# Optimization experiments

Measured on AMD Instinct MI355X. Metric: run time of the kernel, lower is better.

Reference implementation:

```python
import jax, jax.numpy as jnp
import numpy as np


def _grid_sample_2d(feat, gx, gy):
    """Bilinear grid sample, zeros padding, align_corners=False.
    feat: [B,C,H,W]; gx,gy: [B,S,h,w] normalized coords in [-1,1].
    Returns [B,C,S,h,w]. Matches torch 5D grid_sample with D=1, z=0
    (z pixel coord = (1*1-1)/2 = 0 -> weight 1 on the single depth slice).
    """
    B, C, H, W = feat.shape
    ix = ((gx + 1.0) * W - 1.0) * 0.5  # unnormalize, align_corners=False
    iy = ((gy + 1.0) * H - 1.0) * 0.5
    x0 = jnp.floor(ix)
    y0 = jnp.floor(iy)
    tx = ix - x0  # fractional parts (differentiable w.r.t. grid)
    ty = iy - y0
    x0i = x0.astype(jnp.int32)
    y0i = y0.astype(jnp.int32)
    feat_flat = feat.reshape(B, C, H * W)

    def gather(xi, yi):
        valid = (xi >= 0) & (xi < W) & (yi >= 0) & (yi < H)
        xc = jnp.clip(xi, 0, W - 1)
        yc = jnp.clip(yi, 0, H - 1)
        idx = (yc * W + xc).reshape(B, 1, -1)  # [B,1,S*h*w]
        g = jnp.take_along_axis(feat_flat, idx, axis=2)  # [B,C,S*h*w]
        g = g.reshape(B, C, *xi.shape[1:])  # [B,C,S,h,w]
        return g * valid.astype(feat.dtype)[:, None]

    v00 = gather(x0i, y0i)
    v01 = gather(x0i + 1, y0i)
    v10 = gather(x0i, y0i + 1)
    v11 = gather(x0i + 1, y0i + 1)
    w00 = ((1.0 - tx) * (1.0 - ty))[:, None]
    w01 = (tx * (1.0 - ty))[:, None]
    w10 = ((1.0 - tx) * ty)[:, None]
    w11 = (tx * ty)[:, None]
    return v00 * w00 + v01 * w01 + v10 * w10 + v11 * w11


def setup_inputs() -> dict:
    key = jax.random.key(0)
    k1, k2, k3, k4 = jax.random.split(key, 4)
    B, C, S, H, W = 8, 8, 16, 128, 416
    feat_l = jax.random.normal(k1, (B, C, H, W), dtype=jnp.float32)
    feat_r = jax.random.normal(k2, (B, C, H, W), dtype=jnp.float32)
    # LUT: x,y normalized coords (slightly beyond [-1,1] to exercise zero padding);
    # z channel fixed to 0 exactly as in the module's lut_batch construction.
    lut_xy = jax.random.uniform(k3, (B, S, H, W, 2), dtype=jnp.float32,
                                minval=-1.1, maxval=1.1)
    lut = jnp.concatenate([lut_xy, jnp.zeros((B, S, H, W, 1), jnp.float32)], axis=-1)
    valid_mask = jax.random.bernoulli(k4, 0.8, (B, C, S, H, W))
    return {"feat_l": feat_l, "feat_r": feat_r, "lut": lut,
            "valid_mask": valid_mask, "no_steps": S}


def reference(feat_l, feat_r, lut, valid_mask, no_steps):
    """AnyNet._build_volume_2d: LUT grid_sample warp + masked inf-fill
    + abs-diff + channel-sum cost volume. Returns [B, no_steps, H, W]."""
    gx = lut[..., 0]  # torch grid order: (x, y, z), x indexes width
    gy = lut[..., 1]
    warped = _grid_sample_2d(feat_r, gx, gy)          # [B,C,S,H,W]
    diff = jnp.abs(warped - feat_l[:, :, None])       # broadcast feat_l over S
    cost_disp_feat = jnp.where(valid_mask, diff, jnp.inf)
    cost_volume = jnp.sum(cost_disp_feat, axis=1)     # [B,S,H,W]
    return cost_volume
```

## Files before the change

### kernel.cpp

```cpp
#include <hip/hip_runtime.h>
#include <math.h>

#define BB 8
#define CC 8
#define SS 16
#define HH 128
#define WW 416
#define HWSZ (HH * WW)

typedef unsigned short u16;
typedef unsigned char  u8;
typedef unsigned int   u32;
typedef unsigned short ushort8 __attribute__((ext_vector_type(8)));
typedef unsigned int   u32x4   __attribute__((ext_vector_type(4)));
typedef unsigned int   u32x2   __attribute__((ext_vector_type(2)));
typedef float          f32x2   __attribute__((ext_vector_type(2)));
typedef u32x4 __attribute__((aligned(4))) u32x4_a4;

__device__ __forceinline__ float bf2f(u16 v) {
    union { unsigned int u; float f; } x;
    x.u = ((unsigned int)v) << 16;
    return x.f;
}

__device__ __forceinline__ u16 f2bf(float f) {
    union { float ff; unsigned int u; } x;
    x.ff = f;
    unsigned int lsb = (x.u >> 16) & 1u;
    return (u16)((x.u + 0x7FFFu + lsb) >> 16);
}

__device__ __forceinline__ f32x2 bfpair(u32 w) {
    union { u32 u; float f; } lo, hi;
    lo.u = w << 16;
    hi.u = w & 0xFFFF0000u;
    f32x2 r; r.x = lo.f; r.y = hi.f;
    return r;
}

template<bool H>
__device__ __forceinline__ f32x2 fp8pair(u32 w) {
    return (f32x2)__builtin_amdgcn_cvt_pk_f32_fp8(w, H);
}

__device__ __forceinline__ u32 nz_flags(u32 w) {
    return (((w & 0x7F7F7F7Fu) + 0x7F7F7F7Fu) | w) & 0x80808080u;
}

__global__ __launch_bounds__(256) void pack_feats(
    const u16* __restrict__ feat_r,
    const u16* __restrict__ feat_l,
    u32x2* __restrict__ pr8,
    ushort8* __restrict__ pl)
{
    const int idx = blockIdx.x * 256 + threadIdx.x;
    const int b = idx / HWSZ;
    const int p = idx - b * HWSZ;
    const size_t base = (size_t)b * CC * HWSZ + p;

    float fr[CC];
    ushort8 vl;
#pragma unroll
    for (int c = 0; c < CC; ++c) {
        fr[c] = bf2f(__builtin_nontemporal_load(&feat_r[base + (size_t)c * HWSZ]));
        vl[c] = __builtin_nontemporal_load(&feat_l[base + (size_t)c * HWSZ]);
    }
    u32x2 o;
    int w0 = 0, w1 = 0;
    w0 = __builtin_amdgcn_cvt_pk_fp8_f32(fr[0], fr[1], w0, false);
    w0 = __builtin_amdgcn_cvt_pk_fp8_f32(fr[2], fr[3], w0, true);
    w1 = __builtin_amdgcn_cvt_pk_fp8_f32(fr[4], fr[5], w1, false);
    w1 = __builtin_amdgcn_cvt_pk_fp8_f32(fr[6], fr[7], w1, true);
    o.x = (u32)w0; o.y = (u32)w1;
    pr8[idx] = o;
    pl[idx] = vl;
}

__global__ __launch_bounds__(256) void mask_reduce(
    const u8* __restrict__ vmask,
    u8* __restrict__ pmask)
{
    const int t = blockIdx.x * 256 + threadIdx.x;
    const int n16 = SS * HWSZ / 16;
    const int b = t / n16;
    const int r = t - b * n16;
    const u32x4* __restrict__ vm4 = (const u32x4*)vmask;

    u32x4 f = { 0x80808080u, 0x80808080u, 0x80808080u, 0x80808080u };
#pragma unroll
    for (int c = 0; c < CC; ++c) {
        const u32x4 v = __builtin_nontemporal_load(
            &vm4[(size_t)(b * CC + c) * n16 + r]);
        f.x &= nz_flags(v.x);
        f.y &= nz_flags(v.y);
        f.z &= nz_flags(v.z);
        f.w &= nz_flags(v.w);
    }
    __builtin_nontemporal_store(f, &((u32x4*)pmask)[t]);
}

__global__ __launch_bounds__(256) void anynet_cost_volume(
    const u8* __restrict__ pfr8,
    const ushort8* __restrict__ pfl,
    const u16* __restrict__ lut,
    const u8*  __restrict__ pmask,
    u16* __restrict__ out)
{
    const int id = blockIdx.x;
    const int b  = id & 7;
    const int r  = id >> 3;
    const int hwblk = r % (HWSZ / 256);
    const int s     = r / (HWSZ / 256);
    const int hw = hwblk * 256 + (int)threadIdx.x;
    const size_t sp = (size_t)(b * SS + s) * HWSZ + hw;

    const size_t loff = sp * 3;
    const float gx = bf2f(__builtin_nontemporal_load(&lut[loff + 0]));
    const float gy = bf2f(__builtin_nontemporal_load(&lut[loff + 1]));
    const u8 m = __builtin_nontemporal_load(&pmask[sp]);

    const float ix = gx * (0.5f * WW) + (0.5f * WW - 0.5f);
    const float iy = gy * (0.5f * HH) + (0.5f * HH - 0.5f);
    const float x0f = floorf(ix);
    const float y0f = floorf(iy);
    const float tx = ix - x0f;
    const float ty = iy - y0f;
    const int x0 = (int)x0f;
    const int y0 = (int)y0f;
    const int x1 = x0 + 1;
    const int y1 = y0 + 1;

    const bool vx0 = ((unsigned)x0 < (unsigned)WW);
    const bool vx1 = ((unsigned)x1 < (unsigned)WW);
    const bool vy0 = ((unsigned)y0 < (unsigned)HH);
    const bool vy1 = ((unsigned)y1 < (unsigned)HH);

    const int yc0 = min(max(y0, 0), HH - 1);
    const int yc1 = min(max(y1, 0), HH - 1);
    const int bx  = min(max(x0, 0), WW - 2);

    float w00 = (1.0f - tx) * (1.0f - ty) * ((vx0 && vy0) ? 1.0f : 0.0f);
    float w01 = tx * (1.0f - ty)          * ((vx1 && vy0) ? 1.0f : 0.0f);
    float w10 = (1.0f - tx) * ty          * ((vx0 && vy1) ? 1.0f : 0.0f);
    float w11 = tx * ty                   * ((vx1 && vy1) ? 1.0f : 0.0f);

    const bool sw = (x0 == bx);
    const float wl0 = sw ? w00 : w01, wh0 = sw ? w01 : w00;
    const float wl1 = sw ? w10 : w11, wh1 = sw ? w11 : w10;

    const u8* __restrict__ imb = pfr8 + (size_t)b * HWSZ * 8;
    const u32x4 r0 = *(const u32x4_a4*)(imb + 8 * (size_t)(yc0 * WW + bx));
    const u32x4 r1 = *(const u32x4_a4*)(imb + 8 * (size_t)(yc1 * WW + bx));

    union { ushort8 sv; u32x4 w; } flu;
    flu.sv = pfl[(size_t)b * HWSZ + hw];

    f32x2 acc2; acc2.x = 0.0f; acc2.y = 0.0f;
#define CHPAIR(K, WSEL, HSEL)                                              \
    {                                                                      \
        f32x2 wv = fp8pair<HSEL>(WSEL ? r0.y : r0.x) * wl0;                \
        wv += fp8pair<HSEL>(WSEL ? r0.w : r0.z) * wh0;                     \
        wv += fp8pair<HSEL>(WSEL ? r1.y : r1.x) * wl1;                     \
        wv += fp8pair<HSEL>(WSEL ? r1.w : r1.z) * wh1;                     \
        const f32x2 d = wv - bfpair(flu.w[K]);                             \
        f32x2 ad; ad.x = fabsf(d.x); ad.y = fabsf(d.y);                    \
        acc2 += ad;                                                        \
    }
    CHPAIR(0, 0, false)
    CHPAIR(1, 0, true)
    CHPAIR(2, 1, false)
    CHPAIR(3, 1, true)
#undef CHPAIR
    float acc = acc2.x + acc2.y;

    acc = fminf(fmaxf(acc, 0.0f), 1e30f);
    if (!(acc >= 0.0f && acc <= 1e30f)) acc = 0.0f;
    __builtin_nontemporal_store((m == 0) ? (u16)0x7F7F : f2bf(acc), &out[sp]);
}

extern "C" void kernel_launch(void* const* d_in, const int* in_sizes, int n_in,
                              void* d_out, int out_size, void* d_ws, size_t ws_size,
                              hipStream_t stream) {
    const u16* feat_l = (const u16*)d_in[0];
    const u16* feat_r = (const u16*)d_in[1];
    const u16* lut    = (const u16*)d_in[2];
    const u8*  vmask  = (const u8*)d_in[3];
    u16* out = (u16*)d_out;

    u32x2* pfr8 = (u32x2*)d_ws;
    ushort8* pfl = (ushort8*)(pfr8 + (size_t)BB * HWSZ);
    u8* pmask = (u8*)(pfl + (size_t)BB * HWSZ);

    pack_feats<<<dim3(BB * HWSZ / 256), dim3(256), 0, stream>>>(
        feat_r, feat_l, pfr8, pfl);
    mask_reduce<<<dim3(BB * SS * HWSZ / 16 / 256), dim3(256), 0, stream>>>(
        vmask, pmask);

    anynet_cost_volume<<<dim3(BB * SS * (HWSZ / 256)), dim3(256), 0, stream>>>(
        (const u8*)pfr8, pfl, lut, pmask, out);
}
```

Before: 336.2 us.

## Fuse mask reduction and feat_l packing into the cost-volume kernel

Drops the separate mask_reduce kernel and the feat_l packing step, so the main kernel reads the per-channel valid mask and bf16 feat_l directly. This removes the intermediate packed-mask and packed-feat_l buffers and one kernel launch. The cost is byte-wide and strided per-channel loads in the main kernel instead of single vector loads.

```diff
diff --git a/kernel.cpp b/kernel.cpp
--- a/kernel.cpp
+++ b/kernel.cpp
@@ -30,28 +30,14 @@
     return (u16)((x.u + 0x7FFFu + lsb) >> 16);
 }
 
-__device__ __forceinline__ f32x2 bfpair(u32 w) {
-    union { u32 u; float f; } lo, hi;
-    lo.u = w << 16;
-    hi.u = w & 0xFFFF0000u;
-    f32x2 r; r.x = lo.f; r.y = hi.f;
-    return r;
-}
-
 template<bool H>
 __device__ __forceinline__ f32x2 fp8pair(u32 w) {
     return (f32x2)__builtin_amdgcn_cvt_pk_f32_fp8(w, H);
 }
 
-__device__ __forceinline__ u32 nz_flags(u32 w) {
-    return (((w & 0x7F7F7F7Fu) + 0x7F7F7F7Fu) | w) & 0x80808080u;
-}
-
-__global__ __launch_bounds__(256) void pack_feats(
+__global__ __launch_bounds__(256) void pack_feat_r8(
     const u16* __restrict__ feat_r,
-    const u16* __restrict__ feat_l,
-    u32x2* __restrict__ pr8,
-    ushort8* __restrict__ pl)
+    u32x2* __restrict__ pr8)
 {
     const int idx = blockIdx.x * 256 + threadIdx.x;
     const int b = idx / HWSZ;
@@ -59,12 +45,10 @@
     const size_t base = (size_t)b * CC * HWSZ + p;
 
     float fr[CC];
-    ushort8 vl;
 #pragma unroll
-    for (int c = 0; c < CC; ++c) {
+    for (int c = 0; c < CC; ++c)
         fr[c] = bf2f(__builtin_nontemporal_load(&feat_r[base + (size_t)c * HWSZ]));
-        vl[c] = __builtin_nontemporal_load(&feat_l[base + (size_t)c * HWSZ]);
-    }
+
     u32x2 o;
     int w0 = 0, w1 = 0;
     w0 = __builtin_amdgcn_cvt_pk_fp8_f32(fr[0], fr[1], w0, false);
@@ -73,37 +57,13 @@
     w1 = __builtin_amdgcn_cvt_pk_fp8_f32(fr[6], fr[7], w1, true);
     o.x = (u32)w0; o.y = (u32)w1;
     pr8[idx] = o;
-    pl[idx] = vl;
-}
-
-__global__ __launch_bounds__(256) void mask_reduce(
-    const u8* __restrict__ vmask,
-    u8* __restrict__ pmask)
-{
-    const int t = blockIdx.x * 256 + threadIdx.x;
-    const int n16 = SS * HWSZ / 16;
-    const int b = t / n16;
-    const int r = t - b * n16;
-    const u32x4* __restrict__ vm4 = (const u32x4*)vmask;
-
-    u32x4 f = { 0x80808080u, 0x80808080u, 0x80808080u, 0x80808080u };
-#pragma unroll
-    for (int c = 0; c < CC; ++c) {
-        const u32x4 v = __builtin_nontemporal_load(
-            &vm4[(size_t)(b * CC + c) * n16 + r]);
-        f.x &= nz_flags(v.x);
-        f.y &= nz_flags(v.y);
-        f.z &= nz_flags(v.z);
-        f.w &= nz_flags(v.w);
-    }
-    __builtin_nontemporal_store(f, &((u32x4*)pmask)[t]);
 }
 
 __global__ __launch_bounds__(256) void anynet_cost_volume(
     const u8* __restrict__ pfr8,
-    const ushort8* __restrict__ pfl,
+    const u16* __restrict__ feat_l,
     const u16* __restrict__ lut,
-    const u8*  __restrict__ pmask,
+    const u8*  __restrict__ vmask,
     u16* __restrict__ out)
 {
     const int id = blockIdx.x;
@@ -117,7 +77,18 @@
     const size_t loff = sp * 3;
     const float gx = bf2f(__builtin_nontemporal_load(&lut[loff + 0]));
     const float gy = bf2f(__builtin_nontemporal_load(&lut[loff + 1]));
-    const u8 m = __builtin_nontemporal_load(&pmask[sp]);
+
+    const u8* __restrict__ vm = vmask + ((size_t)(b * CC) * SS + s) * HWSZ + hw;
+    bool any_invalid = false;
+#pragma unroll
+    for (int c = 0; c < CC; ++c)
+        any_invalid |= (__builtin_nontemporal_load(&vm[(size_t)c * SS * HWSZ]) == 0);
+
+    const size_t lbase = (size_t)b * CC * HWSZ + hw;
+    u16 flv[CC];
+#pragma unroll
+    for (int c = 0; c < CC; ++c)
+        flv[c] = feat_l[lbase + (size_t)c * HWSZ];
 
     const float ix = gx * (0.5f * WW) + (0.5f * WW - 0.5f);
     const float iy = gy * (0.5f * HH) + (0.5f * HH - 0.5f);
@@ -139,10 +110,10 @@
     const int yc1 = min(max(y1, 0), HH - 1);
     const int bx  = min(max(x0, 0), WW - 2);
 
-    float w00 = (1.0f - tx) * (1.0f - ty) * ((vx0 && vy0) ? 1.0f : 0.0f);
-    float w01 = tx * (1.0f - ty)          * ((vx1 && vy0) ? 1.0f : 0.0f);
-    float w10 = (1.0f - tx) * ty          * ((vx0 && vy1) ? 1.0f : 0.0f);
-    float w11 = tx * ty                   * ((vx1 && vy1) ? 1.0f : 0.0f);
+    const float w00 = (1.0f - tx) * (1.0f - ty) * ((vx0 && vy0) ? 1.0f : 0.0f);
+    const float w01 = tx * (1.0f - ty)          * ((vx1 && vy0) ? 1.0f : 0.0f);
+    const float w10 = (1.0f - tx) * ty          * ((vx0 && vy1) ? 1.0f : 0.0f);
+    const float w11 = tx * ty                   * ((vx1 && vy1) ? 1.0f : 0.0f);
 
     const bool sw = (x0 == bx);
     const float wl0 = sw ? w00 : w01, wh0 = sw ? w01 : w00;
@@ -152,9 +123,6 @@
     const u32x4 r0 = *(const u32x4_a4*)(imb + 8 * (size_t)(yc0 * WW + bx));
     const u32x4 r1 = *(const u32x4_a4*)(imb + 8 * (size_t)(yc1 * WW + bx));
 
-    union { ushort8 sv; u32x4 w; } flu;
-    flu.sv = pfl[(size_t)b * HWSZ + hw];
-
     f32x2 acc2; acc2.x = 0.0f; acc2.y = 0.0f;
 #define CHPAIR(K, WSEL, HSEL)                                              \
     {                                                                      \
@@ -162,7 +130,8 @@
         wv += fp8pair<HSEL>(WSEL ? r0.w : r0.z) * wh0;                     \
         wv += fp8pair<HSEL>(WSEL ? r1.y : r1.x) * wl1;                     \
         wv += fp8pair<HSEL>(WSEL ? r1.w : r1.z) * wh1;                     \
-        const f32x2 d = wv - bfpair(flu.w[K]);                             \
+        f32x2 fl; fl.x = bf2f(flv[2*(K)]); fl.y = bf2f(flv[2*(K)+1]);      \
+        const f32x2 d = wv - fl;                                           \
         f32x2 ad; ad.x = fabsf(d.x); ad.y = fabsf(d.y);                    \
         acc2 += ad;                                                        \
     }
@@ -175,7 +144,7 @@
 
     acc = fminf(fmaxf(acc, 0.0f), 1e30f);
     if (!(acc >= 0.0f && acc <= 1e30f)) acc = 0.0f;
-    __builtin_nontemporal_store((m == 0) ? (u16)0x7F7F : f2bf(acc), &out[sp]);
+    __builtin_nontemporal_store(any_invalid ? (u16)0x7F7F : f2bf(acc), &out[sp]);
 }
 
 extern "C" void kernel_launch(void* const* d_in, const int* in_sizes, int n_in,
@@ -188,14 +157,9 @@
     u16* out = (u16*)d_out;
 
     u32x2* pfr8 = (u32x2*)d_ws;
-    ushort8* pfl = (ushort8*)(pfr8 + (size_t)BB * HWSZ);
-    u8* pmask = (u8*)(pfl + (size_t)BB * HWSZ);
 
-    pack_feats<<<dim3(BB * HWSZ / 256), dim3(256), 0, stream>>>(
-        feat_r, feat_l, pfr8, pfl);
-    mask_reduce<<<dim3(BB * SS * HWSZ / 16 / 256), dim3(256), 0, stream>>>(
-        vmask, pmask);
+    pack_feat_r8<<<dim3(BB * HWSZ / 256), dim3(256), 0, stream>>>(feat_r, pfr8);
 
     anynet_cost_volume<<<dim3(BB * SS * (HWSZ / 256)), dim3(256), 0, stream>>>(
-        (const u8*)pfr8, pfl, lut, pmask, out);
+        (const u8*)pfr8, feat_l, lut, vmask, out);
 }
```

New measurement: 330.8 us. No clear change (-1.6%).
